# Optimization experiments

Measured on AMD Instinct MI355X. Metric: run time of the kernel, lower is better.

## Reference

```python
import jax, jax.numpy as jnp
import numpy as np

B, T, HID = 4, 2048, 1024
H, D = 16, 64  # num_heads, depth = hidden // heads
NEG_INF = -1e9


def setup_inputs() -> dict:
    key = jax.random.key(0)
    ks = jax.random.split(key, 8)
    s = 1.0 / np.sqrt(HID)
    return {
        "q": jax.random.normal(ks[0], (B, T, HID), jnp.float32),
        "k": jax.random.normal(ks[1], (B, T, HID), jnp.float32),
        "v": jax.random.normal(ks[2], (B, T, HID), jnp.float32),
        "pad_mask": jax.random.randint(ks[3], (B, T), 0, 2, jnp.int32),
        "Wq": jax.random.normal(ks[4], (HID, HID), jnp.float32) * s,
        "Wk": jax.random.normal(ks[5], (HID, HID), jnp.float32) * s,
        "Wv": jax.random.normal(ks[6], (HID, HID), jnp.float32) * s,
        "Wo": jax.random.normal(ks[7], (HID, HID), jnp.float32) * s,
    }


def _split_heads(x):
    # [B, T, HID] -> [B*H, T, D]
    b, t, _ = x.shape
    return x.reshape(b, t, H, D).transpose(0, 2, 1, 3).reshape(b * H, t, D)


def _combine_heads(x):
    # [B*H, T, D] -> [B, T, HID]
    t = x.shape[1]
    return x.reshape(-1, H, t, D).transpose(0, 2, 1, 3).reshape(-1, t, HID)


def reference(q, k, v, pad_mask, Wq, Wk, Wv, Wo):
    qp = _split_heads(q @ Wq) * (D ** -0.5)   # [B*H, Tq, D]
    kp = _split_heads(k @ Wk)                  # [B*H, Tk, D]
    vp = _split_heads(v @ Wv)                  # [B*H, Tk, D]
    # additive pad bias: repeat([H,1]) is head-major tiling, reproduced via jnp.tile
    bias = jnp.tile(pad_mask.astype(jnp.float32) * NEG_INF, (H, 1))[:, None, :]
    logits = jnp.einsum('bqd,bkd->bqk', qp, kp) + bias  # [B*H, Tq, Tk]
    weights = jax.nn.softmax(logits, axis=-1)
    # original calls functional.dropout but discards the result -> no-op
    out = jnp.einsum('bqk,bkd->bqd', weights, vp)
    out = _combine_heads(out)                  # [B, Tq, HID]
    return out @ Wo
```

## Files before the change

kernel.cpp:

```cpp
#include <hip/hip_runtime.h>
#include <hip/hip_bf16.h>

#define TQ 2048
#define HIDDEN 1024
#define NB 4
#define NH 16
#define DH 64
#define BHN (NB*NH)
#define LOG2E 1.44269504f

typedef __attribute__((ext_vector_type(4))) float f32x4;
typedef __attribute__((ext_vector_type(8))) short s16x8;

#if __has_builtin(__builtin_amdgcn_exp2f)
#define EXP2(x) __builtin_amdgcn_exp2f(x)
#else
#define EXP2(x) exp2f(x)
#endif

__device__ inline unsigned short f2bf(float f) {
    union { float f; unsigned int u; } x; x.f = f;
    unsigned int r = x.u + 0x7fffu + ((x.u >> 16) & 1u);
    return (unsigned short)(r >> 16);
}

__device__ inline unsigned int pkbf(float a, float b) {
    __hip_bfloat162 h = __float22bfloat162_rn(make_float2(a, b));
    return *reinterpret_cast<unsigned int*>(&h);
}

union PBU { uint4 u4; s16x8 v; };

#define GLL16(gsrc, ldst) \
    __builtin_amdgcn_global_load_lds( \
        (const __attribute__((address_space(1))) unsigned int*)(gsrc), \
        (__attribute__((address_space(3))) unsigned int*)(ldst), 16, 0, 0)

__global__ __launch_bounds__(256) void wt_kernel(const float* W0, const float* W1,
                                                 const float* W2, const float* W3,
                                                 unsigned short* Wt,
                                                 const int* __restrict__ pad,
                                                 unsigned short* __restrict__ maskAndB) {
    if (blockIdx.z == 4) {
        int lin = blockIdx.y * 16 + blockIdx.x;
        if (lin < 32) {
            int p = lin * 256 + threadIdx.x;
            int r = p >> 11, off = p & 2047;
            int o6 = off & 63;
            int ks = o6 >> 5, k32 = o6 & 31;
            int lg = k32 >> 3, j = k32 & 7;
            int key = (off & ~63) | (ks * 32 + ((j >> 2) << 4) + (lg << 2) + (j & 3));
            maskAndB[p] = pad[r * 2048 + key] ? (unsigned short)0 : (unsigned short)0xFFFF;
        }
        return;
    }
    const float* W = (blockIdx.z == 0) ? W0 : (blockIdx.z == 1) ? W1
                    : (blockIdx.z == 2) ? W2 : W3;
    unsigned short* out = Wt + (size_t)blockIdx.z * HIDDEN * HIDDEN;
    __shared__ float tile[64][68];
    int t = threadIdx.x;
    int k0 = blockIdx.y * 64, n0 = blockIdx.x * 64;
#pragma unroll
    for (int i = 0; i < 4; i++) {
        int r = (t >> 4) + i * 16;
        int c = (t & 15) * 4;
        float4 v = *(const float4*)(W + (size_t)(k0 + r) * HIDDEN + n0 + c);
        tile[r][c] = v.x; tile[r][c+1] = v.y; tile[r][c+2] = v.z; tile[r][c+3] = v.w;
    }
    __syncthreads();
#pragma unroll
    for (int i = 0; i < 4; i++) {
        int n = (t >> 4) + i * 16;
        int kc = (t & 15) * 4;
        ushort4 o;
        o.x = f2bf(tile[kc+0][n]); o.y = f2bf(tile[kc+1][n]);
        o.z = f2bf(tile[kc+2][n]); o.w = f2bf(tile[kc+3][n]);
        *(ushort4*)(out + (size_t)(n0 + n) * HIDDEN + k0 + kc) = o;
    }
}

__global__ __launch_bounds__(256) void gemm_proj(const float* __restrict__ A,
                                                 const unsigned short* __restrict__ Bt,
                                                 unsigned short* __restrict__ outb,
                                                 float scale, int vt) {
    __shared__ alignas(16) float As[128 * 64];
    __shared__ alignas(16) unsigned short Bs[128 * 64];
    const int t = threadIdx.x;
    const int wave = t >> 6, lane = t & 63;
    const int wr = wave >> 1, wc = wave & 1;
    const int lr = lane & 15, lg = lane >> 4;
    const int linear = blockIdx.x + 8 * blockIdx.y;
    const int tile = ((linear & 7) << 6) | (linear >> 3);
    const int m0 = (tile >> 3) * 128, n0 = (tile & 7) * 128;

    size_t gA[8];
#pragma unroll
    for (int i = 0; i < 8; i++) {
        int f = i * 256 + t;
        int row = f >> 4, sg = (f & 15) ^ (row & 15);
        gA[i] = (size_t)(m0 + row) * HIDDEN + sg * 4;
    }
    size_t gB[4];
#pragma unroll
    for (int i = 0; i < 4; i++) {
        int f = i * 256 + t;
        int row = f >> 3, sg = (f & 7) ^ (row & 7);
        gB[i] = (size_t)(n0 + row) * HIDDEN + sg * 8;
    }

    f32x4 acc[4][4] = {};

    for (int k0 = 0; k0 < HIDDEN; k0 += 64) {
        __syncthreads();
#pragma unroll
        for (int i = 0; i < 8; i++)
            GLL16(A + gA[i] + k0, &As[(size_t)(i * 256 + wave * 64) * 4]);
#pragma unroll
        for (int i = 0; i < 4; i++)
            GLL16(Bt + gB[i] + k0, &Bs[(size_t)(i * 256 + wave * 64) * 8]);
        __syncthreads();
#pragma unroll
        for (int q = 0; q < 2; q++) {
            s16x8 af[4], bfr[4];
#pragma unroll
            for (int mi = 0; mi < 4; mi++) {
                int row = wr * 64 + mi * 16 + lr;
                int s0 = (q * 8 + lg * 2) ^ (row & 15);
                int s1 = (q * 8 + lg * 2 + 1) ^ (row & 15);
                float4 a0 = *(const float4*)(&As[row * 64 + s0 * 4]);
                float4 a1 = *(const float4*)(&As[row * 64 + s1 * 4]);
                PBU u;
                u.u4.x = pkbf(a0.x, a0.y); u.u4.y = pkbf(a0.z, a0.w);
                u.u4.z = pkbf(a1.x, a1.y); u.u4.w = pkbf(a1.z, a1.w);
                af[mi] = u.v;
            }
#pragma unroll
            for (int ni = 0; ni < 4; ni++) {
                int row = wc * 64 + ni * 16 + lr;
                int s = (q * 4 + lg) ^ (row & 7);
                bfr[ni] = *(const s16x8*)(&Bs[row * 64 + s * 8]);
            }
#pragma unroll
            for (int mi = 0; mi < 4; mi++)
#pragma unroll
                for (int ni = 0; ni < 4; ni++)
                    acc[mi][ni] = __builtin_amdgcn_mfma_f32_16x16x32_bf16(af[mi], bfr[ni], acc[mi][ni], 0, 0, 0);
        }
    }

    if (vt == 0) {
#pragma unroll
        for (int mi = 0; mi < 4; mi++)
#pragma unroll
            for (int ni = 0; ni < 4; ni++)
#pragma unroll
                for (int j = 0; j < 4; j++) {
                    int m = m0 + wr * 64 + mi * 16 + lg * 4 + j;
                    int n = n0 + wc * 64 + ni * 16 + lr;
                    int b = m >> 11, tt = m & (TQ - 1);
                    int h = n >> 6, d = n & 63;
                    outb[((size_t)(b * NH + h) * TQ + tt) * DH + d] = f2bf(acc[mi][ni][j] * scale);
                }
    } else {
#pragma unroll
        for (int mi = 0; mi < 4; mi++)
#pragma unroll
            for (int ni = 0; ni < 4; ni++) {
                int m = m0 + wr * 64 + mi * 16 + lg * 4;
                int n = n0 + wc * 64 + ni * 16 + lr;
                int b = m >> 11, tt = m & (TQ - 1);
                int h = n >> 6, d = n & 63;
                ushort4 pk;
                pk.x = f2bf(acc[mi][ni][0] * scale);
                pk.y = f2bf(acc[mi][ni][1] * scale);
                pk.z = f2bf(acc[mi][ni][2] * scale);
                pk.w = f2bf(acc[mi][ni][3] * scale);
                *(ushort4*)(outb + ((size_t)(b * NH + h) * DH + d) * TQ + tt) = pk;
            }
    }
}

__global__ __launch_bounds__(256) void gemm_out(const unsigned short* __restrict__ A,
                                                const unsigned short* __restrict__ Bt,
                                                float* __restrict__ out) {
    __shared__ alignas(16) unsigned short As[128 * 64];
    __shared__ alignas(16) unsigned short Bs[128 * 64];
    const int t = threadIdx.x;
    const int wave = t >> 6, lane = t & 63;
    const int wr = wave >> 1, wc = wave & 1;
    const int lr = lane & 15, lg = lane >> 4;
    const int linear = blockIdx.x + 8 * blockIdx.y;
    const int tile = ((linear & 7) << 6) | (linear >> 3);
    const int m0 = (tile >> 3) * 128, n0 = (tile & 7) * 128;

    size_t gA[4], gB[4];
#pragma unroll
    for (int i = 0; i < 4; i++) {
        int f = i * 256 + t;
        int row = f >> 3, sg = (f & 7) ^ (row & 7);
        gA[i] = (size_t)(m0 + row) * HIDDEN + sg * 8;
        gB[i] = (size_t)(n0 + row) * HIDDEN + sg * 8;
    }

    f32x4 acc[4][4] = {};

    for (int k0 = 0; k0 < HIDDEN; k0 += 64) {
        __syncthreads();
#pragma unroll
        for (int i = 0; i < 4; i++) {
            GLL16(A + gA[i] + k0, &As[(size_t)(i * 256 + wave * 64) * 8]);
            GLL16(Bt + gB[i] + k0, &Bs[(size_t)(i * 256 + wave * 64) * 8]);
        }
        __syncthreads();
#pragma unroll
        for (int q = 0; q < 2; q++) {
            s16x8 af[4], bfr[4];
#pragma unroll
            for (int mi = 0; mi < 4; mi++) {
                int row = wr * 64 + mi * 16 + lr;
                int s = (q * 4 + lg) ^ (row & 7);
                af[mi] = *(const s16x8*)(&As[row * 64 + s * 8]);
            }
#pragma unroll
            for (int ni = 0; ni < 4; ni++) {
                int row = wc * 64 + ni * 16 + lr;
                int s = (q * 4 + lg) ^ (row & 7);
                bfr[ni] = *(const s16x8*)(&Bs[row * 64 + s * 8]);
            }
#pragma unroll
            for (int mi = 0; mi < 4; mi++)
#pragma unroll
                for (int ni = 0; ni < 4; ni++)
                    acc[mi][ni] = __builtin_amdgcn_mfma_f32_16x16x32_bf16(af[mi], bfr[ni], acc[mi][ni], 0, 0, 0);
        }
    }
#pragma unroll
    for (int mi = 0; mi < 4; mi++)
#pragma unroll
        for (int ni = 0; ni < 4; ni++)
#pragma unroll
            for (int j = 0; j < 4; j++) {
                int m = m0 + wr * 64 + mi * 16 + lg * 4 + j;
                int n = n0 + wc * 64 + ni * 16 + lr;
                out[(size_t)m * HIDDEN + n] = acc[mi][ni][j];
            }
}

__global__ __launch_bounds__(256, 2) void attn_kernel(
        const unsigned short* __restrict__ QP,
        const unsigned short* __restrict__ KP,
        const unsigned short* __restrict__ VT,
        const unsigned short* __restrict__ maskAndB,
        unsigned short* __restrict__ AO) {
    __shared__ alignas(16) unsigned short Ks[2][64 * 72];
    __shared__ alignas(16) unsigned short Vs[2][64 * 72];
    const int t = threadIdx.x, wave = t >> 6, lane = t & 63;
    const int lr = lane & 15, lg = lane >> 4;
    const int linear = blockIdx.x + 8 * blockIdx.y;
    const int bh = ((linear & 7) << 3) | ((linear >> 3) & 7);
    const int qb = linear >> 6;
    const int q0 = qb * 256 + wave * 64;
    const unsigned short* Qb = QP + (size_t)bh * TQ * DH;
    const unsigned short* Kb = KP + (size_t)bh * TQ * DH;
    const unsigned short* Vb = VT + (size_t)bh * DH * TQ;
    const unsigned short* mrow = maskAndB + (bh & (NB - 1)) * TQ;

    const short ob = (short)0x3F80;
    const s16x8 ones = {ob, ob, ob, ob, ob, ob, ob, ob};

    s16x8 qf[4][2];
#pragma unroll
    for (int u = 0; u < 4; u++)
#pragma unroll
        for (int hh = 0; hh < 2; hh++)
            qf[u][hh] = *(const s16x8*)(Qb + (size_t)(q0 + u * 16 + lr) * DH + hh * 32 + lg * 8);

    const int c0 = t, c1 = 256 + t;
    const int sr0 = c0 >> 3, scl0 = (c0 & 7) * 8;
    const int sr1 = c1 >> 3, scl1 = (c1 & 7) * 8;
    const unsigned short* kA0 = Kb + sr0 * DH + scl0;
    const unsigned short* kA1 = Kb + sr1 * DH + scl1;
    const unsigned short* vA0 = Vb + (size_t)sr0 * TQ + scl0;
    const unsigned short* vA1 = Vb + (size_t)sr1 * TQ + scl1;
    const int ksO0 = sr0 * 72 + scl0, ksO1 = sr1 * 72 + scl1;
    const int cc0 = c0 & 7, cc1 = c1 & 7;
    const int vg0 = ((cc0 & 4) << 1) + ((cc0 & 1) << 2) + ((cc0 >> 1) & 1);
    const int vg1 = ((cc1 & 4) << 1) + ((cc1 & 1) << 2) + ((cc1 >> 1) & 1);
    const int vO0 = sr0 * 72 + vg0 * 4, vO1 = sr1 * 72 + vg1 * 4;

    uint4 kr0, kr1, vr0, vr1;
#define LOAD_TILE(kt_) do { \
        kr0 = *(const uint4*)(kA0 + (size_t)(kt_) * 4096); \
        kr1 = *(const uint4*)(kA1 + (size_t)(kt_) * 4096); \
        vr0 = *(const uint4*)(vA0 + (size_t)(kt_) * 64); \
        vr1 = *(const uint4*)(vA1 + (size_t)(kt_) * 64); \
    } while (0)
#define STORE_TILE(b_) do { \
        *(uint4*)(&Ks[b_][ksO0]) = kr0; \
        *(uint4*)(&Ks[b_][ksO1]) = kr1; \
        *(uint2*)(&Vs[b_][vO0])     = make_uint2(vr0.x, vr0.y); \
        *(uint2*)(&Vs[b_][vO0 + 8]) = make_uint2(vr0.z, vr0.w); \
        *(uint2*)(&Vs[b_][vO1])     = make_uint2(vr1.x, vr1.y); \
        *(uint2*)(&Vs[b_][vO1 + 8]) = make_uint2(vr1.z, vr1.w); \
    } while (0)

    f32x4 o[4][4] = {};
    f32x4 osum[4] = {};

    LOAD_TILE(0);
    STORE_TILE(0);

    const int NT = TQ / 64;
    for (int kt = 0; kt < NT; kt++) {
        __syncthreads();
        const int cur = kt & 1;
        if (kt + 1 < NT) LOAD_TILE(kt + 1);
        uint4 ma0 = *(const uint4*)(mrow + kt * 64 + lg * 8);
        uint4 ma1 = *(const uint4*)(mrow + kt * 64 + 32 + lg * 8);

        f32x4 z[4][4] = {};
#pragma unroll
        for (int ni = 0; ni < 4; ni++) {
            s16x8 kf0 = *(const s16x8*)(&Ks[cur][(ni * 16 + lr) * 72 + lg * 8]);
            s16x8 kf1 = *(const s16x8*)(&Ks[cur][(ni * 16 + lr) * 72 + 32 + lg * 8]);
#pragma unroll
            for (int u = 0; u < 4; u++) {
                z[u][ni] = __builtin_amdgcn_mfma_f32_16x16x32_bf16(kf0, qf[u][0], z[u][ni], 0, 0, 0);
                z[u][ni] = __builtin_amdgcn_mfma_f32_16x16x32_bf16(kf1, qf[u][1], z[u][ni], 0, 0, 0);
            }
        }

        PBU pb[4][2];
#pragma unroll
        for (int u = 0; u < 4; u++) {
#pragma unroll
            for (int ni = 0; ni < 4; ni++)
#pragma unroll
                for (int rr = 0; rr < 4; rr++)
                    z[u][ni][rr] = EXP2(z[u][ni][rr]);
#pragma unroll
            for (int ks = 0; ks < 2; ks++) {
                pb[u][ks].u4.x = pkbf(z[u][2 * ks][0], z[u][2 * ks][1]);
                pb[u][ks].u4.y = pkbf(z[u][2 * ks][2], z[u][2 * ks][3]);
                pb[u][ks].u4.z = pkbf(z[u][2 * ks + 1][0], z[u][2 * ks + 1][1]);
                pb[u][ks].u4.w = pkbf(z[u][2 * ks + 1][2], z[u][2 * ks + 1][3]);
            }
            pb[u][0].u4.x &= ma0.x; pb[u][0].u4.y &= ma0.y;
            pb[u][0].u4.z &= ma0.z; pb[u][0].u4.w &= ma0.w;
            pb[u][1].u4.x &= ma1.x; pb[u][1].u4.y &= ma1.y;
            pb[u][1].u4.z &= ma1.z; pb[u][1].u4.w &= ma1.w;
        }

#pragma unroll
        for (int di = 0; di < 4; di++)
#pragma unroll
            for (int ks = 0; ks < 2; ks++) {
                s16x8 vf = *(const s16x8*)(&Vs[cur][(di * 16 + lr) * 72 + ks * 32 + lg * 8]);
#pragma unroll
                for (int u = 0; u < 4; u++)
                    o[u][di] = __builtin_amdgcn_mfma_f32_16x16x32_bf16(vf, pb[u][ks].v, o[u][di], 0, 0, 0);
            }
#pragma unroll
        for (int u = 0; u < 4; u++) {
            osum[u] = __builtin_amdgcn_mfma_f32_16x16x32_bf16(ones, pb[u][0].v, osum[u], 0, 0, 0);
            osum[u] = __builtin_amdgcn_mfma_f32_16x16x32_bf16(ones, pb[u][1].v, osum[u], 0, 0, 0);
        }

        if (kt + 1 < NT) STORE_TILE((kt + 1) & 1);
    }

    const int b = bh >> 4, h = bh & 15;
#pragma unroll
    for (int u = 0; u < 4; u++) {
        float inv = 1.f / osum[u][0];
        int tt = q0 + u * 16 + lr;
#pragma unroll
        for (int di = 0; di < 4; di++) {
            uint2 w;
            w.x = pkbf(o[u][di][0] * inv, o[u][di][1] * inv);
            w.y = pkbf(o[u][di][2] * inv, o[u][di][3] * inv);
            *(uint2*)(AO + (size_t)(b * TQ + tt) * HIDDEN + h * 64 + di * 16 + lg * 4) = w;
        }
    }
#undef LOAD_TILE
#undef STORE_TILE
}

extern "C" void kernel_launch(void* const* d_in, const int* in_sizes, int n_in,
                              void* d_out, int out_size, void* d_ws, size_t ws_size,
                              hipStream_t stream) {
    const float* q  = (const float*)d_in[0];
    const float* k  = (const float*)d_in[1];
    const float* v  = (const float*)d_in[2];
    const int* pad  = (const int*)d_in[3];
    const float* Wq = (const float*)d_in[4];
    const float* Wk = (const float*)d_in[5];
    const float* Wv = (const float*)d_in[6];
    const float* Wo = (const float*)d_in[7];
    float* out = (float*)d_out;

    unsigned short* ws = (unsigned short*)d_ws;
    unsigned short* Wt = ws;
    unsigned short* AO = ws + (size_t)4 * 1024 * 1024;
    unsigned short* QP = AO + (size_t)BHN * TQ * DH;
    unsigned short* KP = QP + (size_t)BHN * TQ * DH;
    unsigned short* VTb = KP + (size_t)BHN * TQ * DH;
    unsigned short* maskAndB = VTb + (size_t)BHN * TQ * DH;
    (void)ws_size; (void)in_sizes; (void)n_in; (void)out_size;

    dim3 b256(256);
    const dim3 gGemm(8, 64);
    wt_kernel<<<dim3(16, 16, 5), b256, 0, stream>>>(Wq, Wk, Wv, Wo, Wt, pad, maskAndB);
    gemm_proj<<<gGemm, b256, 0, stream>>>(q, Wt + (size_t)0 * 1024 * 1024, QP, 0.125f * LOG2E, 0);
    gemm_proj<<<gGemm, b256, 0, stream>>>(k, Wt + (size_t)1 * 1024 * 1024, KP, 1.0f, 0);
    gemm_proj<<<gGemm, b256, 0, stream>>>(v, Wt + (size_t)2 * 1024 * 1024, VTb, 1.0f, 1);
    attn_kernel<<<gGemm, b256, 0, stream>>>(QP, KP, VTb, maskAndB, AO);
    gemm_out<<<gGemm, b256, 0, stream>>>(AO, Wt + (size_t)3 * 1024 * 1024, out);
}
```

Measured before the change: 195.8 us.

## Split attention key range across two wave groups per block with LDS reduction

Doubles the attention block to 512 threads, with two 4-wave groups each processing half of the key/value sequence using separate double-buffered LDS tiles. At the end, the second group writes its partial output and row sums to shared memory, and the first group combines them, normalizes and writes the result. This is meant to raise wave occupancy and shorten each wave's serial key loop. The cost is a larger LDS footprint, a reduction step, and a tighter register budget from the new launch bounds.

```diff
diff --git a/kernel.cpp b/kernel.cpp
--- a/kernel.cpp
+++ b/kernel.cpp
@@ -246,24 +246,24 @@
             }
 }
 
-__global__ __launch_bounds__(256, 2) void attn_kernel(
+__global__ __launch_bounds__(512, 4) void attn_kernel(
         const unsigned short* __restrict__ QP,
         const unsigned short* __restrict__ KP,
         const unsigned short* __restrict__ VT,
         const unsigned short* __restrict__ maskAndB,
         unsigned short* __restrict__ AO) {
-    __shared__ alignas(16) unsigned short Ks[2][64 * 72];
-    __shared__ alignas(16) unsigned short Vs[2][64 * 72];
+    __shared__ alignas(16) unsigned short SM[8 * 64 * 72];
     const int t = threadIdx.x, wave = t >> 6, lane = t & 63;
+    const int grp = wave >> 2, wv = wave & 3;
     const int lr = lane & 15, lg = lane >> 4;
     const int linear = blockIdx.x + 8 * blockIdx.y;
     const int bh = ((linear & 7) << 3) | ((linear >> 3) & 7);
     const int qb = linear >> 6;
-    const int q0 = qb * 256 + wave * 64;
+    const int q0 = qb * 256 + wv * 64;
     const unsigned short* Qb = QP + (size_t)bh * TQ * DH;
-    const unsigned short* Kb = KP + (size_t)bh * TQ * DH;
+    const unsigned short* Kb = KP + (size_t)bh * TQ * DH + (size_t)grp * 1024 * DH;
     const unsigned short* Vb = VT + (size_t)bh * DH * TQ;
-    const unsigned short* mrow = maskAndB + (bh & (NB - 1)) * TQ;
+    const unsigned short* mrow = maskAndB + (bh & (NB - 1)) * TQ + grp * 1024;
 
     const short ob = (short)0x3F80;
     const s16x8 ones = {ob, ob, ob, ob, ob, ob, ob, ob};
@@ -275,18 +275,24 @@
         for (int hh = 0; hh < 2; hh++)
             qf[u][hh] = *(const s16x8*)(Qb + (size_t)(q0 + u * 16 + lr) * DH + hh * 32 + lg * 8);
 
-    const int c0 = t, c1 = 256 + t;
+    const int st = t & 255;
+    const int c0 = st, c1 = 256 + st;
     const int sr0 = c0 >> 3, scl0 = (c0 & 7) * 8;
     const int sr1 = c1 >> 3, scl1 = (c1 & 7) * 8;
     const unsigned short* kA0 = Kb + sr0 * DH + scl0;
     const unsigned short* kA1 = Kb + sr1 * DH + scl1;
-    const unsigned short* vA0 = Vb + (size_t)sr0 * TQ + scl0;
-    const unsigned short* vA1 = Vb + (size_t)sr1 * TQ + scl1;
+    const unsigned short* vA0 = Vb + (size_t)sr0 * TQ + grp * 1024 + scl0;
+    const unsigned short* vA1 = Vb + (size_t)sr1 * TQ + grp * 1024 + scl1;
     const int ksO0 = sr0 * 72 + scl0, ksO1 = sr1 * 72 + scl1;
     const int cc0 = c0 & 7, cc1 = c1 & 7;
     const int vg0 = ((cc0 & 4) << 1) + ((cc0 & 1) << 2) + ((cc0 >> 1) & 1);
     const int vg1 = ((cc1 & 4) << 1) + ((cc1 & 1) << 2) + ((cc1 >> 1) & 1);
     const int vO0 = sr0 * 72 + vg0 * 4, vO1 = sr1 * 72 + vg1 * 4;
+
+    unsigned short* Kt0 = SM + (size_t)((grp << 1) | 0) * 4608;
+    unsigned short* Kt1 = SM + (size_t)((grp << 1) | 1) * 4608;
+    unsigned short* Vt0 = SM + (size_t)(4 + ((grp << 1) | 0)) * 4608;
+    unsigned short* Vt1 = SM + (size_t)(4 + ((grp << 1) | 1)) * 4608;
 
     uint4 kr0, kr1, vr0, vr1;
 #define LOAD_TILE(kt_) do { \
@@ -296,12 +302,14 @@
         vr1 = *(const uint4*)(vA1 + (size_t)(kt_) * 64); \
     } while (0)
 #define STORE_TILE(b_) do { \
-        *(uint4*)(&Ks[b_][ksO0]) = kr0; \
-        *(uint4*)(&Ks[b_][ksO1]) = kr1; \
-        *(uint2*)(&Vs[b_][vO0])     = make_uint2(vr0.x, vr0.y); \
-        *(uint2*)(&Vs[b_][vO0 + 8]) = make_uint2(vr0.z, vr0.w); \
-        *(uint2*)(&Vs[b_][vO1])     = make_uint2(vr1.x, vr1.y); \
-        *(uint2*)(&Vs[b_][vO1 + 8]) = make_uint2(vr1.z, vr1.w); \
+        unsigned short* kd = (b_) ? Kt1 : Kt0; \
+        unsigned short* vd = (b_) ? Vt1 : Vt0; \
+        *(uint4*)(&kd[ksO0]) = kr0; \
+        *(uint4*)(&kd[ksO1]) = kr1; \
+        *(uint2*)(&vd[vO0])     = make_uint2(vr0.x, vr0.y); \
+        *(uint2*)(&vd[vO0 + 8]) = make_uint2(vr0.z, vr0.w); \
+        *(uint2*)(&vd[vO1])     = make_uint2(vr1.x, vr1.y); \
+        *(uint2*)(&vd[vO1 + 8]) = make_uint2(vr1.z, vr1.w); \
     } while (0)
 
     f32x4 o[4][4] = {};
@@ -310,19 +318,21 @@
     LOAD_TILE(0);
     STORE_TILE(0);
 
-    const int NT = TQ / 64;
+    const int NT = 1024 / 64;
     for (int kt = 0; kt < NT; kt++) {
         __syncthreads();
         const int cur = kt & 1;
         if (kt + 1 < NT) LOAD_TILE(kt + 1);
         uint4 ma0 = *(const uint4*)(mrow + kt * 64 + lg * 8);
         uint4 ma1 = *(const uint4*)(mrow + kt * 64 + 32 + lg * 8);
+        const unsigned short* Kh = cur ? Kt1 : Kt0;
+        const unsigned short* Vh = cur ? Vt1 : Vt0;
 
         f32x4 z[4][4] = {};
 #pragma unroll
         for (int ni = 0; ni < 4; ni++) {
-            s16x8 kf0 = *(const s16x8*)(&Ks[cur][(ni * 16 + lr) * 72 + lg * 8]);
-            s16x8 kf1 = *(const s16x8*)(&Ks[cur][(ni * 16 + lr) * 72 + 32 + lg * 8]);
+            s16x8 kf0 = *(const s16x8*)(&Kh[(ni * 16 + lr) * 72 + lg * 8]);
+            s16x8 kf1 = *(const s16x8*)(&Kh[(ni * 16 + lr) * 72 + 32 + lg * 8]);
 #pragma unroll
             for (int u = 0; u < 4; u++) {
                 z[u][ni] = __builtin_amdgcn_mfma_f32_16x16x32_bf16(kf0, qf[u][0], z[u][ni], 0, 0, 0);
@@ -355,7 +365,7 @@
         for (int di = 0; di < 4; di++)
 #pragma unroll
             for (int ks = 0; ks < 2; ks++) {
-                s16x8 vf = *(const s16x8*)(&Vs[cur][(di * 16 + lr) * 72 + ks * 32 + lg * 8]);
+                s16x8 vf = *(const s16x8*)(&Vh[(di * 16 + lr) * 72 + ks * 32 + lg * 8]);
 #pragma unroll
                 for (int u = 0; u < 4; u++)
                     o[u][di] = __builtin_amdgcn_mfma_f32_16x16x32_bf16(vf, pb[u][ks].v, o[u][di], 0, 0, 0);
@@ -369,17 +379,38 @@
         if (kt + 1 < NT) STORE_TILE((kt + 1) & 1);
     }
 
-    const int b = bh >> 4, h = bh & 15;
-#pragma unroll
-    for (int u = 0; u < 4; u++) {
-        float inv = 1.f / osum[u][0];
-        int tt = q0 + u * 16 + lr;
-#pragma unroll
-        for (int di = 0; di < 4; di++) {
-            uint2 w;
-            w.x = pkbf(o[u][di][0] * inv, o[u][di][1] * inv);
-            w.y = pkbf(o[u][di][2] * inv, o[u][di][3] * inv);
-            *(uint2*)(AO + (size_t)(b * TQ + tt) * HIDDEN + h * 64 + di * 16 + lg * 4) = w;
+    __syncthreads();
+    float* cb = (float*)SM;
+    const int cbase = (wv * 64 + lane) * 68;
+    if (grp == 1) {
+#pragma unroll
+        for (int u = 0; u < 4; u++) {
+#pragma unroll
+            for (int di = 0; di < 4; di++)
+                *(float4*)(cb + cbase + u * 16 + di * 4) =
+                    make_float4(o[u][di][0], o[u][di][1], o[u][di][2], o[u][di][3]);
+        }
+        float4 sv = make_float4(osum[0][0], osum[1][0], osum[2][0], osum[3][0]);
+        *(float4*)(cb + cbase + 64) = sv;
+    }
+    __syncthreads();
+    if (grp == 0) {
+        const int b = bh >> 4, h = bh & 15;
+        float4 sv = *(const float4*)(cb + cbase + 64);
+        float stot[4] = {osum[0][0] + sv.x, osum[1][0] + sv.y,
+                         osum[2][0] + sv.z, osum[3][0] + sv.w};
+#pragma unroll
+        for (int u = 0; u < 4; u++) {
+            float inv = 1.f / stot[u];
+            int tt = q0 + u * 16 + lr;
+#pragma unroll
+            for (int di = 0; di < 4; di++) {
+                float4 p = *(const float4*)(cb + cbase + u * 16 + di * 4);
+                uint2 w;
+                w.x = pkbf((o[u][di][0] + p.x) * inv, (o[u][di][1] + p.y) * inv);
+                w.y = pkbf((o[u][di][2] + p.z) * inv, (o[u][di][3] + p.w) * inv);
+                *(uint2*)(AO + (size_t)(b * TQ + tt) * HIDDEN + h * 64 + di * 16 + lg * 4) = w;
+            }
         }
     }
 #undef LOAD_TILE
@@ -414,6 +445,6 @@
     gemm_proj<<<gGemm, b256, 0, stream>>>(q, Wt + (size_t)0 * 1024 * 1024, QP, 0.125f * LOG2E, 0);
     gemm_proj<<<gGemm, b256, 0, stream>>>(k, Wt + (size_t)1 * 1024 * 1024, KP, 1.0f, 0);
     gemm_proj<<<gGemm, b256, 0, stream>>>(v, Wt + (size_t)2 * 1024 * 1024, VTb, 1.0f, 1);
-    attn_kernel<<<gGemm, b256, 0, stream>>>(QP, KP, VTb, maskAndB, AO);
+    attn_kernel<<<gGemm, dim3(512), 0, stream>>>(QP, KP, VTb, maskAndB, AO);
     gemm_out<<<gGemm, b256, 0, stream>>>(AO, Wt + (size_t)3 * 1024 * 1024, out);
 }
```

Result: slower. 628.3 us (+220.8%).
